# Performance work log

Hardware: AMD Instinct MI355X
Metric: run time of the kernel (lower is better)

Reference implementation:

```python
import jax, jax.numpy as jnp
import numpy as np

NOISE_STD = 0.1
NUM_EXPERTS = 32
TOPK = 2
OUTPUT_DIM = 256


def setup_inputs() -> dict:
    key = jax.random.key(0)
    k_x, k_n, k_gw, k_ew = jax.random.split(key, 4)
    N, D_IN = 32768, 256
    E, D_OUT = NUM_EXPERTS, OUTPUT_DIM
    x = jax.random.normal(k_x, (N, D_IN), dtype=jnp.float32)
    noise = jax.random.normal(k_n, (N, E), dtype=jnp.float32)
    # gate: nn.Linear(input_dim, num_experts) default init scale
    gate_w = jax.random.normal(k_gw, (E, D_IN), dtype=jnp.float32) / jnp.sqrt(D_IN).astype(jnp.float32)
    gate_b = jnp.zeros((E,), dtype=jnp.float32)
    # experts: nn.Linear(input_dim, output_dim * num_experts), xavier_uniform weight, zero bias
    lim = float(np.sqrt(6.0 / (D_IN + D_OUT * E)))
    experts_w = jax.random.uniform(k_ew, (D_OUT * E, D_IN), minval=-lim, maxval=lim, dtype=jnp.float32)
    experts_b = jnp.zeros((D_OUT * E,), dtype=jnp.float32)
    return {"x": x, "noise": noise, "gate_w": gate_w, "gate_b": gate_b,
            "experts_w": experts_w, "experts_b": experts_b}


def reference(x, noise, gate_w, gate_b, experts_w, experts_b):
    N = x.shape[0]
    E, D = NUM_EXPERTS, OUTPUT_DIM
    # gating with noisy logits
    gate_logits = x @ gate_w.T + gate_b + noise * NOISE_STD          # [N, E]
    gate_probs = jax.nn.softmax(gate_logits, axis=-1)                # [N, E]
    # load-balance auxiliary loss
    gate_probs_mean = gate_probs.mean(axis=0)                        # [E]
    expected = 1.0 / E
    load_balance_loss = jnp.mean((gate_probs_mean - expected) ** 2) * E
    # top-k routing
    topk_probs, topk_idx = jax.lax.top_k(gate_probs, TOPK)           # [N, k]
    # all-expert dense linear, then gather the selected experts
    expert_outputs = (x @ experts_w.T + experts_b).reshape(N, E, D)  # [N, E, D]
    sel = jnp.take_along_axis(expert_outputs, topk_idx[:, :, None], axis=1)  # [N, k, D]
    output = jnp.einsum('bk,bkd->bd', topk_probs, sel)               # [N, D]
    return output, load_balance_loss
```

## Files before the change

### kernel.cpp

```cpp
#include <hip/hip_runtime.h>
#include <hip/hip_bf16.h>

#define N_ROWS 32768
#define D_INP  256
#define NEXP   32
#define D_OUTP 256
#define TROWS  64
#define NTILES 1056
#define GROWS  64

typedef __attribute__((ext_vector_type(4))) float f32x4;
typedef __attribute__((ext_vector_type(8))) short bf16x8;

__device__ inline unsigned short f2b(float f) {
    union { __hip_bfloat16 h; unsigned short u; } cv;
    cv.h = __float2bfloat16(f);
    return cv.u;
}
__device__ inline float b2f(unsigned short u) {
    union { unsigned v; float f; } c; c.v = ((unsigned)u) << 16; return c.f;
}

__global__ __launch_bounds__(256) void gate_kernel(
    const float* __restrict__ x, const float* __restrict__ noise,
    const float* __restrict__ gw, const float* __restrict__ gb,
    const float* __restrict__ ew, unsigned short* __restrict__ wbT,
    unsigned short* __restrict__ xb, float* __restrict__ tkp,
    int* __restrict__ tki, float* __restrict__ esum, int* __restrict__ ecnt)
{
    __shared__ float gws[NEXP * 260];
    __shared__ float xs[GROWS * 132];
    __shared__ float lsum[NEXP];
    __shared__ int   lcnt[NEXP];

    int tid = threadIdx.x;
    int row0 = blockIdx.x * GROWS;

    #pragma unroll
    for (int it = 0; it < 8; ++it) {
        int q = it * 256 + tid;
        int e = q >> 6;
        int k = (q & 63) * 4;
        float4 v = ((const float4*)gw)[q];
        *(float4*)&gws[e * 260 + k] = v;
    }
    if (tid < NEXP) { lsum[tid] = 0.f; lcnt[tid] = 0; }

    int e4 = tid & 7;
    int rq = tid >> 3;

    float acc[2][4];
    #pragma unroll
    for (int m = 0; m < 2; m++)
        #pragma unroll
        for (int n = 0; n < 4; n++) acc[m][n] = 0.f;

    for (int h = 0; h < 2; ++h) {
        int ko = h * 128;
        __syncthreads();
        #pragma unroll
        for (int it = 0; it < 8; ++it) {
            int idx = it * 256 + tid;
            int r = idx >> 5;
            int f = idx & 31;
            float4 v = *(const float4*)(x + (size_t)(row0 + r) * D_INP + ko + f * 4);
            *(float4*)&xs[r * 132 + f * 4] = v;
            unsigned short b[4] = { f2b(v.x), f2b(v.y), f2b(v.z), f2b(v.w) };
            *(ushort4*)(xb + (size_t)(row0 + r) * D_INP + ko + f * 4) = *(ushort4*)b;
        }
        __syncthreads();
        #pragma unroll 4
        for (int c = 0; c < 32; ++c) {
            float4 xv[2], wv[4];
            #pragma unroll
            for (int m = 0; m < 2; m++)
                xv[m] = *(float4*)&xs[(rq + 32 * m) * 132 + c * 4];
            #pragma unroll
            for (int n = 0; n < 4; n++)
                wv[n] = *(float4*)&gws[(e4 + 8 * n) * 260 + ko + c * 4];
            #pragma unroll
            for (int m = 0; m < 2; m++)
                #pragma unroll
                for (int n = 0; n < 4; n++)
                    acc[m][n] = fmaf(xv[m].x, wv[n].x,
                                fmaf(xv[m].y, wv[n].y,
                                fmaf(xv[m].z, wv[n].z,
                                fmaf(xv[m].w, wv[n].w, acc[m][n]))));
        }
    }

    #pragma unroll
    for (int m = 0; m < 2; m++) {
        int R = row0 + rq + 32 * m;
        float l[4], p[4];
        #pragma unroll
        for (int n = 0; n < 4; n++) {
            int E = e4 + 8 * n;
            l[n] = acc[m][n] + gb[E] + 0.1f * noise[(size_t)R * NEXP + E];
        }
        float mx = fmaxf(fmaxf(l[0], l[1]), fmaxf(l[2], l[3]));
        #pragma unroll
        for (int s = 1; s < 8; s <<= 1) mx = fmaxf(mx, __shfl_xor(mx, s));
        float sum = 0.f;
        #pragma unroll
        for (int n = 0; n < 4; n++) { p[n] = expf(l[n] - mx); sum += p[n]; }
        #pragma unroll
        for (int s = 1; s < 8; s <<= 1) sum += __shfl_xor(sum, s);
        float inv = 1.f / sum;
        #pragma unroll
        for (int n = 0; n < 4; n++) p[n] *= inv;

        float bp = p[0]; int bi = e4;
        #pragma unroll
        for (int n = 1; n < 4; n++) if (p[n] > bp) { bp = p[n]; bi = e4 + 8 * n; }
        #pragma unroll
        for (int s = 1; s < 8; s <<= 1) {
            float op = __shfl_xor(bp, s); int oi = __shfl_xor(bi, s);
            if (op > bp || (op == bp && oi < bi)) { bp = op; bi = oi; }
        }
        float bp2 = -1.f; int bi2 = 0;
        #pragma unroll
        for (int n = 0; n < 4; n++) {
            int E = e4 + 8 * n;
            float q = (E == bi) ? -1.f : p[n];
            if (q > bp2 || (q == bp2 && E < bi2)) { bp2 = q; bi2 = E; }
        }
        #pragma unroll
        for (int s = 1; s < 8; s <<= 1) {
            float op = __shfl_xor(bp2, s); int oi = __shfl_xor(bi2, s);
            if (op > bp2 || (op == bp2 && oi < bi2)) { bp2 = op; bi2 = oi; }
        }
        if (e4 == 0) {
            tkp[R * 2] = bp;  tkp[R * 2 + 1] = bp2;
            tki[R * 2] = bi;  tki[R * 2 + 1] = bi2;
            atomicAdd(&lcnt[bi], 1); atomicAdd(&lcnt[bi2], 1);
        }
        #pragma unroll
        for (int n = 0; n < 4; n++) atomicAdd(&lsum[e4 + 8 * n], p[n]);
    }

    #pragma unroll
    for (int it = 0; it < 2; ++it) {
        int fid = blockIdx.x * 512 + it * 256 + tid;
        int row = fid >> 5;
        int kc  = fid & 31;
        const float4* s = (const float4*)(ew + (size_t)row * D_INP + kc * 8);
        float4 v0 = s[0], v1 = s[1];
        unsigned short t[8] = { f2b(v0.x), f2b(v0.y), f2b(v0.z), f2b(v0.w),
                                f2b(v1.x), f2b(v1.y), f2b(v1.z), f2b(v1.w) };
        int e  = row >> 8;
        int rr = row & 255;
        int q  = rr >> 6;
        int nn = (rr >> 4) & 3;
        int lr = rr & 15;
        int kk = kc >> 2;
        int kg = kc & 3;
        size_t off = ((((size_t)(e * 4 + q) * 8 + kk) * 4 + nn) * 64 + kg * 16 + lr) * 8;
        *(uint4*)(wbT + off) = *(uint4*)t;
    }

    __syncthreads();
    if (tid < NEXP) {
        unsafeAtomicAdd(&esum[tid], lsum[tid]);
        atomicAdd(&ecnt[tid], lcnt[tid]);
    }
}

__global__ __launch_bounds__(1024) void build_list_kernel(
    const int* __restrict__ tki, const float* __restrict__ esum,
    const int* __restrict__ ecnt, int* __restrict__ cursor0,
    int* __restrict__ list, float* __restrict__ loss_out)
{
    __shared__ int lcnt[NEXP], lbase[NEXP], s_offs[NEXP + 1];
    int tid = threadIdx.x;
    if (tid < NEXP) lcnt[tid] = 0;
    if (tid < 32) {
        int c = ecnt[tid];
        int ic = c;
        #pragma unroll
        for (int s = 1; s < 32; s <<= 1) {
            int a = __shfl_up(ic, s, 32);
            if (tid >= s) ic += a;
        }
        s_offs[tid + 1] = ic;
        if (tid == 0) s_offs[0] = 0;
    }
    __syncthreads();
    int r = blockIdx.x * 1024 + tid;
    int e0 = tki[r * 2], e1 = tki[r * 2 + 1];
    int p0 = atomicAdd(&lcnt[e0], 1);
    int p1 = atomicAdd(&lcnt[e1], 1);
    __syncthreads();
    if (tid < NEXP) lbase[tid] = s_offs[tid] + atomicAdd(&cursor0[tid], lcnt[tid]);
    __syncthreads();
    list[lbase[e0] + p0] = r * 2;
    list[lbase[e1] + p1] = r * 2 + 1;

    if (blockIdx.x == 0 && tid < 32) {
        float d = esum[tid] * (1.f / N_ROWS) - (1.f / NEXP);
        float v = d * d;
        #pragma unroll
        for (int s = 16; s > 0; s >>= 1) v += __shfl_xor(v, s, 32);
        if (tid == 0) *loss_out = v;
    }
}

__global__ __launch_bounds__(256) void moe_gemm_kernel(
    const unsigned short* __restrict__ xb, const unsigned short* __restrict__ wbT,
    const float* __restrict__ expb, const float* __restrict__ tkp,
    const int* __restrict__ list, const int* __restrict__ ecnt,
    unsigned short* __restrict__ y0, unsigned short* __restrict__ y1)
{
    __shared__ int s_offs[NEXP + 1], s_toff[NEXP + 1];
    __shared__ unsigned short xa[TROWS * 256];
    __shared__ int   srow[TROWS];
    __shared__ int   sslot[TROWS];
    __shared__ float sprob[TROWS];

    int tid = threadIdx.x;
    if (tid < 32) {
        int c = ecnt[tid];
        int ic = c, itc = (c + TROWS - 1) >> 6;
        #pragma unroll
        for (int s = 1; s < 32; s <<= 1) {
            int a  = __shfl_up(ic, s, 32);  if (tid >= s) ic += a;
            int b2 = __shfl_up(itc, s, 32); if (tid >= s) itc += b2;
        }
        s_offs[tid + 1] = ic; s_toff[tid + 1] = itc;
        if (tid == 0) { s_offs[0] = 0; s_toff[0] = 0; }
    }
    __syncthreads();

    int b = (blockIdx.x & 7) * (NTILES / 8) + (blockIdx.x >> 3);
    if (b >= s_toff[NEXP]) return;
    int e = 0;
    #pragma unroll
    for (int s = 16; s; s >>= 1)
        if (e + s <= 31 && s_toff[e + s] <= b) e += s;
    int m0 = s_offs[e] + (b - s_toff[e]) * TROWS;
    int nr = min(TROWS, s_offs[e + 1] - m0);

    if (tid < TROWS) {
        if (tid < nr) {
            int ent = list[m0 + tid];
            srow[tid]  = ent >> 1;
            sslot[tid] = ent & 1;
            sprob[tid] = tkp[ent];
        } else { srow[tid] = -1; sslot[tid] = 0; sprob[tid] = 0.f; }
    }
    __syncthreads();

    {
        int r_ = tid >> 2;
        int gr = srow[r_]; if (gr < 0) gr = 0;
        const uint4* src = (const uint4*)(xb + (size_t)gr * D_INP);
        uint4* dst = (uint4*)xa;
        int swz = r_ & 7;
        #pragma unroll
        for (int i = 0; i < 8; ++i) {
            int c = (tid & 3) + 4 * i;
            dst[r_ * 32 + (c ^ swz)] = src[c];
        }
    }
    __syncthreads();

    int wave = tid >> 6;
    int lane = tid & 63;
    int lr = lane & 15;
    int kg = lane >> 4;
    int n0 = wave * 64;
    int aswz = lr & 7;

    const unsigned short* wbase = wbT + (size_t)(e * 4 + wave) * 32 * 512;

    f32x4 acc[4][4];
    #pragma unroll
    for (int mm = 0; mm < 4; mm++)
        #pragma unroll
        for (int nn = 0; nn < 4; nn++)
            acc[mm][nn] = (f32x4){0.f, 0.f, 0.f, 0.f};

    #pragma unroll
    for (int kk = 0; kk < 8; kk++) {
        int chunk = kk * 4 + kg;
        bf16x8 a[4], bb[4];
        #pragma unroll
        for (int mm = 0; mm < 4; mm++)
            a[mm] = *(const bf16x8*)&xa[(mm * 16 + lr) * 256 + ((chunk ^ aswz) * 8)];
        #pragma unroll
        for (int nn = 0; nn < 4; nn++)
            bb[nn] = *(const bf16x8*)(wbase + (kk * 4 + nn) * 512 + lane * 8);
        #pragma unroll
        for (int mm = 0; mm < 4; mm++)
            #pragma unroll
            for (int nn = 0; nn < 4; nn++)
                acc[mm][nn] = __builtin_amdgcn_mfma_f32_16x16x32_bf16(a[mm], bb[nn], acc[mm][nn], 0, 0, 0);
    }
    __syncthreads();

    {
        float bias[4];
        #pragma unroll
        for (int nn = 0; nn < 4; nn++) bias[nn] = expb[e * 256 + n0 + nn * 16 + lr];
        #pragma unroll
        for (int mm = 0; mm < 4; mm++) {
            #pragma unroll
            for (int j = 0; j < 4; j++) {
                int lrow = mm * 16 + kg * 4 + j;
                float pp = sprob[lrow];
                #pragma unroll
                for (int nn = 0; nn < 4; nn++) {
                    float v = (acc[mm][nn][j] + bias[nn]) * pp;
                    xa[lrow * 256 + n0 + nn * 16 + lr] = f2b(v);
                }
            }
        }
    }
    __syncthreads();

    {
        int r_ = tid >> 2;
        int gr = srow[r_];
        if (gr >= 0) {
            unsigned short* dstb = (sslot[r_] ? y1 : y0) + (size_t)gr * D_OUTP;
            const uint4* src = (const uint4*)(xa + r_ * 256);
            uint4* dst = (uint4*)dstb;
            #pragma unroll
            for (int i = 0; i < 8; ++i) {
                int c = (tid & 3) + 4 * i;
                dst[c] = src[c];
            }
        }
    }
}

__global__ __launch_bounds__(256) void combine_kernel(
    const unsigned short* __restrict__ y0, const unsigned short* __restrict__ y1,
    float* __restrict__ out)
{
    size_t i = ((size_t)blockIdx.x * 256 + threadIdx.x) * 8;
    uint4 a = *(const uint4*)(y0 + i);
    uint4 b = *(const uint4*)(y1 + i);
    const unsigned short* ap = (const unsigned short*)&a;
    const unsigned short* bp = (const unsigned short*)&b;
    float4 o0, o1;
    o0.x = b2f(ap[0]) + b2f(bp[0]);
    o0.y = b2f(ap[1]) + b2f(bp[1]);
    o0.z = b2f(ap[2]) + b2f(bp[2]);
    o0.w = b2f(ap[3]) + b2f(bp[3]);
    o1.x = b2f(ap[4]) + b2f(bp[4]);
    o1.y = b2f(ap[5]) + b2f(bp[5]);
    o1.z = b2f(ap[6]) + b2f(bp[6]);
    o1.w = b2f(ap[7]) + b2f(bp[7]);
    *(float4*)(out + i)     = o0;
    *(float4*)(out + i + 4) = o1;
}

extern "C" void kernel_launch(void* const* d_in, const int* in_sizes, int n_in,
                              void* d_out, int out_size, void* d_ws, size_t ws_size,
                              hipStream_t stream)
{
    const float* x   = (const float*)d_in[0];
    const float* noi = (const float*)d_in[1];
    const float* gw  = (const float*)d_in[2];
    const float* gb  = (const float*)d_in[3];
    const float* ew  = (const float*)d_in[4];
    const float* eb  = (const float*)d_in[5];
    float* out = (float*)d_out;

    char* p = (char*)d_ws;
    unsigned short* xb  = (unsigned short*)p; p += (size_t)N_ROWS * D_INP * 2;
    unsigned short* wbT = (unsigned short*)p; p += (size_t)NEXP * D_OUTP * D_INP * 2;
    unsigned short* y0  = (unsigned short*)p; p += (size_t)N_ROWS * D_OUTP * 2;
    unsigned short* y1  = (unsigned short*)p; p += (size_t)N_ROWS * D_OUTP * 2;
    float* tkp  = (float*)p; p += (size_t)N_ROWS * 2 * 4;
    int*   tki  = (int*)p;   p += (size_t)N_ROWS * 2 * 4;
    int*   list = (int*)p;   p += (size_t)N_ROWS * 2 * 4;
    float* esum = (float*)p; p += 32 * 4;
    int*   ecnt = (int*)p;   p += 32 * 4;
    int*   cur0 = (int*)p;   p += 32 * 4;

    hipMemsetAsync(esum, 0, 3 * 32 * 4, stream);

    gate_kernel<<<N_ROWS / GROWS, 256, 0, stream>>>(x, noi, gw, gb, ew, wbT, xb, tkp, tki, esum, ecnt);
    build_list_kernel<<<N_ROWS / 1024, 1024, 0, stream>>>(tki, esum, ecnt, cur0, list, out + (size_t)N_ROWS * D_OUTP);
    moe_gemm_kernel<<<NTILES, 256, 0, stream>>>(xb, wbT, eb, tkp, list, ecnt, y0, y1);
    combine_kernel<<<N_ROWS * D_OUTP / 8 / 256, 256, 0, stream>>>(y0, y1, out);
}
```

Measured before the change: 153.8 us.

## Halve gate rows per block and split weight conversion into its own kernel

The gate kernel now handles 32 rows per block instead of 64, which doubles the grid to 1024 blocks and cuts per-thread accumulators to one row. The expert weight fp32-to-bf16 transpose moves out of the gate kernel into a separate wtrans_kernel launched with 1024 blocks. The aim is more parallelism and a lighter gate kernel. The cost is an extra launch, and the gate weights are now reloaded into shared memory by twice as many blocks.

```diff
diff --git a/kernel.cpp b/kernel.cpp
--- a/kernel.cpp
+++ b/kernel.cpp
@@ -7,7 +7,7 @@
 #define D_OUTP 256
 #define TROWS  64
 #define NTILES 1056
-#define GROWS  64
+#define GROWS  32
 
 typedef __attribute__((ext_vector_type(4))) float f32x4;
 typedef __attribute__((ext_vector_type(8))) short bf16x8;
@@ -24,7 +24,6 @@
 __global__ __launch_bounds__(256) void gate_kernel(
     const float* __restrict__ x, const float* __restrict__ noise,
     const float* __restrict__ gw, const float* __restrict__ gb,
-    const float* __restrict__ ew, unsigned short* __restrict__ wbT,
     unsigned short* __restrict__ xb, float* __restrict__ tkp,
     int* __restrict__ tki, float* __restrict__ esum, int* __restrict__ ecnt)
 {
@@ -49,17 +48,13 @@
     int e4 = tid & 7;
     int rq = tid >> 3;
 
-    float acc[2][4];
-    #pragma unroll
-    for (int m = 0; m < 2; m++)
-        #pragma unroll
-        for (int n = 0; n < 4; n++) acc[m][n] = 0.f;
+    float acc[4] = {0.f, 0.f, 0.f, 0.f};
 
     for (int h = 0; h < 2; ++h) {
         int ko = h * 128;
         __syncthreads();
         #pragma unroll
-        for (int it = 0; it < 8; ++it) {
+        for (int it = 0; it < 4; ++it) {
             int idx = it * 256 + tid;
             int r = idx >> 5;
             int f = idx & 31;
@@ -71,32 +66,27 @@
         __syncthreads();
         #pragma unroll 4
         for (int c = 0; c < 32; ++c) {
-            float4 xv[2], wv[4];
-            #pragma unroll
-            for (int m = 0; m < 2; m++)
-                xv[m] = *(float4*)&xs[(rq + 32 * m) * 132 + c * 4];
+            float4 xv = *(float4*)&xs[rq * 132 + c * 4];
+            float4 wv[4];
             #pragma unroll
             for (int n = 0; n < 4; n++)
                 wv[n] = *(float4*)&gws[(e4 + 8 * n) * 260 + ko + c * 4];
             #pragma unroll
-            for (int m = 0; m < 2; m++)
-                #pragma unroll
-                for (int n = 0; n < 4; n++)
-                    acc[m][n] = fmaf(xv[m].x, wv[n].x,
-                                fmaf(xv[m].y, wv[n].y,
-                                fmaf(xv[m].z, wv[n].z,
-                                fmaf(xv[m].w, wv[n].w, acc[m][n]))));
-        }
-    }
-
-    #pragma unroll
-    for (int m = 0; m < 2; m++) {
-        int R = row0 + rq + 32 * m;
+            for (int n = 0; n < 4; n++)
+                acc[n] = fmaf(xv.x, wv[n].x,
+                         fmaf(xv.y, wv[n].y,
+                         fmaf(xv.z, wv[n].z,
+                         fmaf(xv.w, wv[n].w, acc[n]))));
+        }
+    }
+
+    {
+        int R = row0 + rq;
         float l[4], p[4];
         #pragma unroll
         for (int n = 0; n < 4; n++) {
             int E = e4 + 8 * n;
-            l[n] = acc[m][n] + gb[E] + 0.1f * noise[(size_t)R * NEXP + E];
+            l[n] = acc[n] + gb[E] + 0.1f * noise[(size_t)R * NEXP + E];
         }
         float mx = fmaxf(fmaxf(l[0], l[1]), fmaxf(l[2], l[3]));
         #pragma unroll
@@ -139,31 +129,32 @@
         for (int n = 0; n < 4; n++) atomicAdd(&lsum[e4 + 8 * n], p[n]);
     }
 
-    #pragma unroll
-    for (int it = 0; it < 2; ++it) {
-        int fid = blockIdx.x * 512 + it * 256 + tid;
-        int row = fid >> 5;
-        int kc  = fid & 31;
-        const float4* s = (const float4*)(ew + (size_t)row * D_INP + kc * 8);
-        float4 v0 = s[0], v1 = s[1];
-        unsigned short t[8] = { f2b(v0.x), f2b(v0.y), f2b(v0.z), f2b(v0.w),
-                                f2b(v1.x), f2b(v1.y), f2b(v1.z), f2b(v1.w) };
-        int e  = row >> 8;
-        int rr = row & 255;
-        int q  = rr >> 6;
-        int nn = (rr >> 4) & 3;
-        int lr = rr & 15;
-        int kk = kc >> 2;
-        int kg = kc & 3;
-        size_t off = ((((size_t)(e * 4 + q) * 8 + kk) * 4 + nn) * 64 + kg * 16 + lr) * 8;
-        *(uint4*)(wbT + off) = *(uint4*)t;
-    }
-
     __syncthreads();
     if (tid < NEXP) {
         unsafeAtomicAdd(&esum[tid], lsum[tid]);
         atomicAdd(&ecnt[tid], lcnt[tid]);
     }
+}
+
+__global__ __launch_bounds__(256) void wtrans_kernel(
+    const float* __restrict__ ew, unsigned short* __restrict__ wbT)
+{
+    int fid = blockIdx.x * 256 + threadIdx.x;
+    int row = fid >> 5;
+    int kc  = fid & 31;
+    const float4* s = (const float4*)(ew + (size_t)row * D_INP + kc * 8);
+    float4 v0 = s[0], v1 = s[1];
+    unsigned short t[8] = { f2b(v0.x), f2b(v0.y), f2b(v0.z), f2b(v0.w),
+                            f2b(v1.x), f2b(v1.y), f2b(v1.z), f2b(v1.w) };
+    int e  = row >> 8;
+    int rr = row & 255;
+    int q  = rr >> 6;
+    int nn = (rr >> 4) & 3;
+    int lr = rr & 15;
+    int kk = kc >> 2;
+    int kg = kc & 3;
+    size_t off = ((((size_t)(e * 4 + q) * 8 + kk) * 4 + nn) * 64 + kg * 16 + lr) * 8;
+    *(uint4*)(wbT + off) = *(uint4*)t;
 }
 
 __global__ __launch_bounds__(1024) void build_list_kernel(
@@ -382,7 +373,8 @@
 
     hipMemsetAsync(esum, 0, 3 * 32 * 4, stream);
 
-    gate_kernel<<<N_ROWS / GROWS, 256, 0, stream>>>(x, noi, gw, gb, ew, wbT, xb, tkp, tki, esum, ecnt);
+    gate_kernel<<<N_ROWS / GROWS, 256, 0, stream>>>(x, noi, gw, gb, xb, tkp, tki, esum, ecnt);
+    wtrans_kernel<<<1024, 256, 0, stream>>>(ew, wbT);
     build_list_kernel<<<N_ROWS / 1024, 1024, 0, stream>>>(tki, esum, ecnt, cur0, list, out + (size_t)N_ROWS * D_OUTP);
     moe_gemm_kernel<<<NTILES, 256, 0, stream>>>(xb, wbT, eb, tkp, list, ecnt, y0, y1);
     combine_kernel<<<N_ROWS * D_OUTP / 8 / 256, 256, 0, stream>>>(y0, y1, out);
```

Measured after the change: 168.4 us. +9.4%, slower.

## Split gate GEMM K across waves and reduce partial logits via shared memory

Applied to the files above, without the earlier changes.

The gate logits GEMM now gives each of the four waves a 16-wide slice of every 64-wide K chunk. Each thread accumulates 8 rows by 4 experts, which raises reuse of the weight registers per x load. Partial sums are written to shared memory (reusing the gate-weight buffer) and summed across waves. Softmax and top-2 then run with 4 threads per row and vectorized noise loads. This adds extra barriers, a shared-memory reduction pass and more registers per thread, in exchange for less LDS traffic in the inner loop.

```diff
diff --git a/kernel.cpp b/kernel.cpp
--- a/kernel.cpp
+++ b/kernel.cpp
@@ -28,8 +28,8 @@
     unsigned short* __restrict__ xb, float* __restrict__ tkp,
     int* __restrict__ tki, float* __restrict__ esum, int* __restrict__ ecnt)
 {
-    __shared__ float gws[NEXP * 260];
-    __shared__ float xs[GROWS * 132];
+    __shared__ float rA[8448];
+    __shared__ float xs[64 * 68];
     __shared__ float lsum[NEXP];
     __shared__ int   lcnt[NEXP];
 
@@ -42,101 +42,123 @@
         int e = q >> 6;
         int k = (q & 63) * 4;
         float4 v = ((const float4*)gw)[q];
-        *(float4*)&gws[e * 260 + k] = v;
+        *(float4*)&rA[e * 260 + k] = v;
     }
     if (tid < NEXP) { lsum[tid] = 0.f; lcnt[tid] = 0; }
 
-    int e4 = tid & 7;
-    int rq = tid >> 3;
-
-    float acc[2][4];
-    #pragma unroll
-    for (int m = 0; m < 2; m++)
+    int lane = tid & 63;
+    int wid  = tid >> 6;
+    int e4 = lane & 7;
+    int rq = lane >> 3;
+
+    float acc[8][4];
+    #pragma unroll
+    for (int m = 0; m < 8; m++)
         #pragma unroll
         for (int n = 0; n < 4; n++) acc[m][n] = 0.f;
 
-    for (int h = 0; h < 2; ++h) {
-        int ko = h * 128;
+    for (int s = 0; s < 4; ++s) {
         __syncthreads();
         #pragma unroll
-        for (int it = 0; it < 8; ++it) {
-            int idx = it * 256 + tid;
-            int r = idx >> 5;
-            int f = idx & 31;
-            float4 v = *(const float4*)(x + (size_t)(row0 + r) * D_INP + ko + f * 4);
-            *(float4*)&xs[r * 132 + f * 4] = v;
+        for (int it = 0; it < 4; ++it) {
+            int q = it * 256 + tid;
+            int r = q >> 4;
+            int kq = q & 15;
+            float4 v = *(const float4*)(x + (size_t)(row0 + r) * D_INP + s * 64 + kq * 4);
+            *(float4*)&xs[r * 68 + kq * 4] = v;
             unsigned short b[4] = { f2b(v.x), f2b(v.y), f2b(v.z), f2b(v.w) };
-            *(ushort4*)(xb + (size_t)(row0 + r) * D_INP + ko + f * 4) = *(ushort4*)b;
+            *(ushort4*)(xb + (size_t)(row0 + r) * D_INP + s * 64 + kq * 4) = *(ushort4*)b;
         }
         __syncthreads();
-        #pragma unroll 4
-        for (int c = 0; c < 32; ++c) {
-            float4 xv[2], wv[4];
-            #pragma unroll
-            for (int m = 0; m < 2; m++)
-                xv[m] = *(float4*)&xs[(rq + 32 * m) * 132 + c * 4];
+        int ko = s * 64 + wid * 16;
+        #pragma unroll
+        for (int c = 0; c < 4; ++c) {
+            float4 wv[4];
             #pragma unroll
             for (int n = 0; n < 4; n++)
-                wv[n] = *(float4*)&gws[(e4 + 8 * n) * 260 + ko + c * 4];
-            #pragma unroll
-            for (int m = 0; m < 2; m++)
+                wv[n] = *(float4*)&rA[(e4 + 8 * n) * 260 + ko + c * 4];
+            #pragma unroll
+            for (int m = 0; m < 8; m++) {
+                float4 xv = *(float4*)&xs[(rq + 8 * m) * 68 + wid * 16 + c * 4];
                 #pragma unroll
                 for (int n = 0; n < 4; n++)
-                    acc[m][n] = fmaf(xv[m].x, wv[n].x,
-                                fmaf(xv[m].y, wv[n].y,
-                                fmaf(xv[m].z, wv[n].z,
-                                fmaf(xv[m].w, wv[n].w, acc[m][n]))));
-        }
-    }
-
-    #pragma unroll
-    for (int m = 0; m < 2; m++) {
-        int R = row0 + rq + 32 * m;
-        float l[4], p[4];
-        #pragma unroll
-        for (int n = 0; n < 4; n++) {
-            int E = e4 + 8 * n;
-            l[n] = acc[m][n] + gb[E] + 0.1f * noise[(size_t)R * NEXP + E];
-        }
-        float mx = fmaxf(fmaxf(l[0], l[1]), fmaxf(l[2], l[3]));
-        #pragma unroll
-        for (int s = 1; s < 8; s <<= 1) mx = fmaxf(mx, __shfl_xor(mx, s));
+                    acc[m][n] = fmaf(xv.x, wv[n].x,
+                                fmaf(xv.y, wv[n].y,
+                                fmaf(xv.z, wv[n].z,
+                                fmaf(xv.w, wv[n].w, acc[m][n]))));
+            }
+        }
+    }
+    __syncthreads();
+
+    {
+        int base = (wid * 64 + lane) * 33;
+        #pragma unroll
+        for (int m = 0; m < 8; m++)
+            #pragma unroll
+            for (int n = 0; n < 4; n++)
+                rA[base + m * 4 + n] = acc[m][n];
+    }
+    __syncthreads();
+
+    {
+        int row = tid >> 2;
+        int eo  = (tid & 3) * 8;
+        int n   = tid & 3;
+        int R = row0 + row;
+        int j = (row >> 3) * 4 + n;
+        int lpb = (row & 7) * 8;
+        float4 nz0 = *(const float4*)(noise + (size_t)R * NEXP + eo);
+        float4 nz1 = *(const float4*)(noise + (size_t)R * NEXP + eo + 4);
+        float nz[8] = { nz0.x, nz0.y, nz0.z, nz0.w, nz1.x, nz1.y, nz1.z, nz1.w };
+        float l[8], p[8];
+        #pragma unroll
+        for (int i = 0; i < 8; i++) {
+            int a = (lpb + i) * 33 + j;
+            float v = rA[a] + rA[2112 + a] + rA[4224 + a] + rA[6336 + a];
+            l[i] = v + gb[eo + i] + 0.1f * nz[i];
+        }
+        float mx = l[0];
+        #pragma unroll
+        for (int i = 1; i < 8; i++) mx = fmaxf(mx, l[i]);
+        mx = fmaxf(mx, __shfl_xor(mx, 1));
+        mx = fmaxf(mx, __shfl_xor(mx, 2));
         float sum = 0.f;
         #pragma unroll
-        for (int n = 0; n < 4; n++) { p[n] = expf(l[n] - mx); sum += p[n]; }
-        #pragma unroll
-        for (int s = 1; s < 8; s <<= 1) sum += __shfl_xor(sum, s);
+        for (int i = 0; i < 8; i++) { p[i] = expf(l[i] - mx); sum += p[i]; }
+        sum += __shfl_xor(sum, 1);
+        sum += __shfl_xor(sum, 2);
         float inv = 1.f / sum;
         #pragma unroll
-        for (int n = 0; n < 4; n++) p[n] *= inv;
-
-        float bp = p[0]; int bi = e4;
-        #pragma unroll
-        for (int n = 1; n < 4; n++) if (p[n] > bp) { bp = p[n]; bi = e4 + 8 * n; }
-        #pragma unroll
-        for (int s = 1; s < 8; s <<= 1) {
-            float op = __shfl_xor(bp, s); int oi = __shfl_xor(bi, s);
+        for (int i = 0; i < 8; i++) p[i] *= inv;
+
+        float bp = p[0]; int bi = eo;
+        #pragma unroll
+        for (int i = 1; i < 8; i++) if (p[i] > bp) { bp = p[i]; bi = eo + i; }
+        #pragma unroll
+        for (int s2 = 1; s2 < 4; s2 <<= 1) {
+            float op = __shfl_xor(bp, s2); int oi = __shfl_xor(bi, s2);
             if (op > bp || (op == bp && oi < bi)) { bp = op; bi = oi; }
         }
         float bp2 = -1.f; int bi2 = 0;
         #pragma unroll
-        for (int n = 0; n < 4; n++) {
-            int E = e4 + 8 * n;
-            float q = (E == bi) ? -1.f : p[n];
+        for (int i = 0; i < 8; i++) {
+            int E = eo + i;
+            float q = (E == bi) ? -1.f : p[i];
             if (q > bp2 || (q == bp2 && E < bi2)) { bp2 = q; bi2 = E; }
         }
         #pragma unroll
-        for (int s = 1; s < 8; s <<= 1) {
-            float op = __shfl_xor(bp2, s); int oi = __shfl_xor(bi2, s);
+        for (int s2 = 1; s2 < 4; s2 <<= 1) {
+            float op = __shfl_xor(bp2, s2); int oi = __shfl_xor(bi2, s2);
             if (op > bp2 || (op == bp2 && oi < bi2)) { bp2 = op; bi2 = oi; }
         }
-        if (e4 == 0) {
+        if ((tid & 3) == 0) {
             tkp[R * 2] = bp;  tkp[R * 2 + 1] = bp2;
             tki[R * 2] = bi;  tki[R * 2 + 1] = bi2;
             atomicAdd(&lcnt[bi], 1); atomicAdd(&lcnt[bi2], 1);
         }
         #pragma unroll
-        for (int n = 0; n < 4; n++) atomicAdd(&lsum[e4 + 8 * n], p[n]);
+        for (int i = 0; i < 8; i++) atomicAdd(&lsum[eo + i], p[i]);
     }
 
     #pragma unroll
@@ -144,8 +166,8 @@
         int fid = blockIdx.x * 512 + it * 256 + tid;
         int row = fid >> 5;
         int kc  = fid & 31;
-        const float4* s = (const float4*)(ew + (size_t)row * D_INP + kc * 8);
-        float4 v0 = s[0], v1 = s[1];
+        const float4* sp = (const float4*)(ew + (size_t)row * D_INP + kc * 8);
+        float4 v0 = sp[0], v1 = sp[1];
         unsigned short t[8] = { f2b(v0.x), f2b(v0.y), f2b(v0.z), f2b(v0.w),
                                 f2b(v1.x), f2b(v1.y), f2b(v1.z), f2b(v1.w) };
         int e  = row >> 8;
```

Result: faster. 149.1 us (-3.1%).
